# Kernel tuning notes

Hardware: AMD Instinct MI355X
Metric: run time of the kernel (lower is better)

The kernel has to match this reference:

```python
import jax, jax.numpy as jnp
import numpy as np

N = 50000      # nodes
E = 800000     # edges (avg degree 16)
D_IN = 128
D_H = 128
D_OUT = 64


def setup_inputs() -> dict:
    key = jax.random.key(0)
    k_x, k_e, k_w1, k_b1, k_w2, k_b2 = jax.random.split(key, 6)
    x = jax.random.normal(k_x, (N, D_IN), dtype=jnp.float32)
    edge_index = jax.random.randint(k_e, (2, E), 0, N, dtype=jnp.int32)
    # Glorot-style init for GCN weights, zero bias (as in PyG GCNConv defaults)
    W1 = jax.random.normal(k_w1, (D_IN, D_H), dtype=jnp.float32) * (1.0 / np.sqrt(D_IN))
    b1 = jnp.zeros((D_H,), dtype=jnp.float32)
    W2 = jax.random.normal(k_w2, (D_H, D_OUT), dtype=jnp.float32) * (1.0 / np.sqrt(D_H))
    b2 = jnp.zeros((D_OUT,), dtype=jnp.float32)
    return {"x": x, "edge_index": edge_index, "W1": W1, "b1": b1, "W2": W2, "b2": b2}


def _gcn_norm(edge_index, n):
    # PyG gcn_norm with add_self_loops=True, edge_weight = 1
    loops = jnp.arange(n, dtype=edge_index.dtype)
    src = jnp.concatenate([edge_index[0], loops])  # [E+N]
    dst = jnp.concatenate([edge_index[1], loops])
    deg = jax.ops.segment_sum(jnp.ones_like(dst, dtype=jnp.float32), dst, num_segments=n)
    dinv = jnp.where(deg > 0, jax.lax.rsqrt(deg), 0.0)
    norm = dinv[src] * dinv[dst]                   # [E+N]
    return src, dst, norm


def _gcn_conv(h, src, dst, norm, W, b, n):
    # transform -> gather source -> scale by symmetric norm -> scatter-add at dst -> bias
    hW = h @ W                                      # [N, F_out]
    msg = hW[src] * norm[:, None]                   # [E+N, F_out]
    agg = jax.ops.segment_sum(msg, dst, num_segments=n)
    return agg + b


def reference(x, edge_index, W1, b1, W2, b2):
    n = x.shape[0]
    src, dst, norm = _gcn_norm(edge_index, n)
    x1 = jax.nn.relu(_gcn_conv(x, src, dst, norm, W1, b1, n))
    x2 = _gcn_conv(x1, src, dst, norm, W2, b2, n)
    return x2
```

## Files before the change

kernel.cpp:

```cpp
#include <hip/hip_runtime.h>

#define CAP  64
#define BN   64
#define NBMAX 1024
#define ECAP 2048
#define P1E  4096

typedef unsigned int uint;
typedef unsigned short ushort;
typedef __attribute__((ext_vector_type(8))) short short8;
typedef __attribute__((ext_vector_type(4))) float f32x4;

__device__ inline ushort f2bf(float f) {
    uint u = __float_as_uint(f);
    return (ushort)((u + 0x7fffu + ((u >> 16) & 1u)) >> 16);
}
__device__ inline uint packbf2(float lo, float hi) {
    return (uint)f2bf(lo) | ((uint)f2bf(hi) << 16);
}
__device__ inline void unpackbf2(uint u, float& lo, float& hi) {
    lo = __uint_as_float(u << 16);
    hi = __uint_as_float(u & 0xffff0000u);
}

__global__ __launch_bounds__(256) void k_zero(uint4* __restrict__ p, int n16) {
    int i = blockIdx.x * 256 + threadIdx.x;
    if (i < n16) p[i] = make_uint4(0, 0, 0, 0);
}

__global__ __launch_bounds__(256) void k_part(const int* __restrict__ esrc,
                                              const int* __restrict__ edst,
                                              int E, int nb,
                                              int* __restrict__ gtail,
                                              uint* __restrict__ ebuf) {
    __shared__ int hist[NBMAX];
    int base_e = blockIdx.x * P1E;
    for (int i = threadIdx.x; i < nb; i += 256) hist[i] = 0;
    __syncthreads();

    int d[16], s[16];
#pragma unroll
    for (int u = 0; u < 16; u++) {
        int e = base_e + u * 256 + threadIdx.x;
        d[u] = (e < E) ? edst[e] : -1;
        s[u] = (e < E) ? esrc[e] : 0;
        if (d[u] >= 0) atomicAdd(&hist[d[u] >> 6], 1);
    }
    __syncthreads();

    for (int i = threadIdx.x; i < nb; i += 256) {
        int h = hist[i];
        hist[i] = (h > 0) ? atomicAdd(&gtail[i], h) : 0;
    }
    __syncthreads();

#pragma unroll
    for (int u = 0; u < 16; u++) {
        if (d[u] >= 0) {
            int b = d[u] >> 6;
            int slot = atomicAdd(&hist[b], 1);
            if (slot < ECAP)
                ebuf[(size_t)b * ECAP + slot] =
                    ((uint)(d[u] & (BN - 1)) << 16) | (uint)s[u];
        }
    }
}

__global__ __launch_bounds__(256) void k_csr(const uint* __restrict__ ebuf,
                                             const int* __restrict__ gtail,
                                             int n,
                                             ushort* __restrict__ colbuf,
                                             int* __restrict__ cnt,
                                             float* __restrict__ dinv) {
    __shared__ ushort cb[BN * CAP];
    __shared__ int cl[BN];
    int b = blockIdx.x;
    int ne = gtail[b];
    if (ne > ECAP) ne = ECAP;
    for (int i = threadIdx.x; i < BN; i += 256) cl[i] = 0;
    __syncthreads();

    const uint* eb = ebuf + (size_t)b * ECAP;
    for (int i = threadIdx.x; i < ne; i += 256) {
        uint pr = eb[i];
        int dloc = pr >> 16;
        int p = atomicAdd(&cl[dloc], 1);
        if (p < CAP) cb[dloc * CAP + p] = (ushort)(pr & 0xffffu);
    }
    __syncthreads();

    int node0 = b * BN;
    for (int i = threadIdx.x; i < BN * CAP / 8; i += 256) {
        int node = node0 + i / (CAP / 8);
        if (node < n)
            ((uint4*)&colbuf[(size_t)node0 * CAP])[i] = ((const uint4*)cb)[i];
    }
    for (int i = threadIdx.x; i < BN; i += 256) {
        int node = node0 + i;
        if (node < n) {
            int c = cl[i];
            dinv[node] = rsqrtf((float)c + 1.0f);
            cnt[node] = (c > CAP) ? CAP : c;
        }
    }
}

__global__ __launch_bounds__(256) void k_wprep(const float* __restrict__ W1,
                                               const float* __restrict__ W2,
                                               ushort* __restrict__ W1t,
                                               ushort* __restrict__ W2t) {
    int i = blockIdx.x * 256 + threadIdx.x;
    if (i < 4 * 128 * 32) {
        int kt = i >> 12;
        int nn = (i >> 5) & 127;
        int ko = i & 31;
        W1t[i] = f2bf(W1[(size_t)(kt * 32 + ko) * 128 + nn]);
    }
    int j = i - 4 * 128 * 32;
    if (j >= 0 && j < 4 * 64 * 32) {
        int kt = j >> 11;
        int nn = (j >> 5) & 63;
        int ko = j & 31;
        W2t[j] = f2bf(W2[(size_t)(kt * 32 + ko) * 64 + nn]);
    }
}

template<int NCOL, bool XF32>
__global__ __launch_bounds__(256) void k_mgemm(const float* __restrict__ Xf,
                                               const ushort* __restrict__ Xh,
                                               const ushort* __restrict__ Wt,
                                               ushort* __restrict__ Yb, int n) {
    __shared__ ushort Ws[4 * NCOL * 32];
    for (int idx = threadIdx.x; idx < 4 * NCOL * 32 / 8; idx += 256)
        ((uint4*)Ws)[idx] = ((const uint4*)Wt)[idx];
    __syncthreads();

    int wid  = threadIdx.x >> 6;
    int l    = threadIdx.x & 63;
    int mrow = l & 15;
    int kgrp = l >> 4;
    int row16 = (blockIdx.x * 4 + wid) * 16;
    int r  = row16 + mrow;
    int rc = (r < n) ? r : (n - 1);

    f32x4 acc[NCOL / 16];
#pragma unroll
    for (int t = 0; t < NCOL / 16; t++) acc[t] = (f32x4){0.f, 0.f, 0.f, 0.f};

#pragma unroll
    for (int kt = 0; kt < 4; kt++) {
        short8 a;
        if (XF32) {
            const float* xp = &Xf[(size_t)rc * 128 + kt * 32 + kgrp * 8];
            float4 x0 = *(const float4*)xp;
            float4 x1 = *(const float4*)(xp + 4);
            a[0] = (short)f2bf(x0.x); a[1] = (short)f2bf(x0.y);
            a[2] = (short)f2bf(x0.z); a[3] = (short)f2bf(x0.w);
            a[4] = (short)f2bf(x1.x); a[5] = (short)f2bf(x1.y);
            a[6] = (short)f2bf(x1.z); a[7] = (short)f2bf(x1.w);
        } else {
            a = *(const short8*)&Xh[(size_t)rc * 128 + kt * 32 + kgrp * 8];
        }
#pragma unroll
        for (int t = 0; t < NCOL / 16; t++) {
            short8 b = *(const short8*)&Ws[((kt * NCOL) + t * 16 + mrow) * 32 + kgrp * 8];
            acc[t] = __builtin_amdgcn_mfma_f32_16x16x32_bf16(a, b, acc[t], 0, 0, 0);
        }
    }

    int orow = row16 + kgrp * 4;
#pragma unroll
    for (int t = 0; t < NCOL / 16; t++) {
#pragma unroll
        for (int q = 0; q < 4; q++) {
            int rr = orow + q;
            if (rr < n) Yb[(size_t)rr * NCOL + t * 16 + mrow] = f2bf(acc[t][q]);
        }
    }
}

__global__ __launch_bounds__(256) void k_agg1(const ushort* __restrict__ Hb,
                                              const int* __restrict__ cntc,
                                              const ushort* __restrict__ colbuf,
                                              const float* __restrict__ dinv,
                                              const float* __restrict__ b1,
                                              ushort* __restrict__ x1b, int n) {
    const int CH = 128, LPG = 16;
    int t    = blockIdx.x * 256 + threadIdx.x;
    int gid  = t / LPG;
    int lane = t % LPG;
    if (gid >= n) return;

    float di = dinv[gid];
    int c = cntc[gid];
    if (c > CAP) c = CAP;

    float acc[8];
#pragma unroll
    for (int k = 0; k < 8; k++) acc[k] = 0.f;

    const ushort* cb = colbuf + (size_t)gid * CAP;
    for (int j = 0; j < c; j += 8) {
        uint4 iv = *(const uint4*)(cb + j);
        int s[8];
        s[0] = iv.x & 0xffff; s[1] = iv.x >> 16;
        s[2] = iv.y & 0xffff; s[3] = iv.y >> 16;
        s[4] = iv.z & 0xffff; s[5] = iv.z >> 16;
        s[6] = iv.w & 0xffff; s[7] = iv.w >> 16;
#pragma unroll
        for (int u = 1; u < 8; u++) if (j + u >= c) s[u] = s[0];
        float w[8];
#pragma unroll
        for (int u = 0; u < 8; u++)
            w[u] = (j + u < c) ? dinv[s[u]] : 0.f;
        uint4 h[8];
#pragma unroll
        for (int u = 0; u < 8; u++)
            h[u] = *(const uint4*)(Hb + (size_t)s[u] * CH + lane * 8);
#pragma unroll
        for (int u = 0; u < 8; u++) {
            float f0, f1;
            unpackbf2(h[u].x, f0, f1); acc[0] += f0 * w[u]; acc[1] += f1 * w[u];
            unpackbf2(h[u].y, f0, f1); acc[2] += f0 * w[u]; acc[3] += f1 * w[u];
            unpackbf2(h[u].z, f0, f1); acc[4] += f0 * w[u]; acc[5] += f1 * w[u];
            unpackbf2(h[u].w, f0, f1); acc[6] += f0 * w[u]; acc[7] += f1 * w[u];
        }
    }

    uint4 aself = *(const uint4*)(Hb + (size_t)gid * CH + lane * 8);
    float sf[8];
    unpackbf2(aself.x, sf[0], sf[1]);
    unpackbf2(aself.y, sf[2], sf[3]);
    unpackbf2(aself.z, sf[4], sf[5]);
    unpackbf2(aself.w, sf[6], sf[7]);

    float4 bb0 = *(const float4*)&b1[lane * 8];
    float4 bb1 = *(const float4*)&b1[lane * 8 + 4];
    float bb[8] = {bb0.x, bb0.y, bb0.z, bb0.w, bb1.x, bb1.y, bb1.z, bb1.w};

    float xv[8];
#pragma unroll
    for (int k = 0; k < 8; k++)
        xv[k] = fmaxf((acc[k] + di * sf[k]) * di + bb[k], 0.f);

    uint up[4] = { packbf2(xv[0], xv[1]), packbf2(xv[2], xv[3]),
                   packbf2(xv[4], xv[5]), packbf2(xv[6], xv[7]) };
    *(uint4*)&x1b[(size_t)gid * CH + lane * 8] = *(uint4*)up;
}

__global__ __launch_bounds__(256) void k_agg2(const ushort* __restrict__ Hb,
                                              const int* __restrict__ cntc,
                                              const ushort* __restrict__ colbuf,
                                              const float* __restrict__ dinv,
                                              const float* __restrict__ b2,
                                              float* __restrict__ out, int n) {
    const int CH = 64, LPG = 8;
    int t    = blockIdx.x * 256 + threadIdx.x;
    int gid  = t / LPG;
    int lane = t % LPG;
    if (gid >= n) return;

    float di = dinv[gid];
    int c = cntc[gid];
    if (c > CAP) c = CAP;

    float acc[8];
#pragma unroll
    for (int k = 0; k < 8; k++) acc[k] = 0.f;

    const ushort* cb = colbuf + (size_t)gid * CAP;
    for (int j = 0; j < c; j += 8) {
        uint4 iv = *(const uint4*)(cb + j);
        int s[8];
        s[0] = iv.x & 0xffff; s[1] = iv.x >> 16;
        s[2] = iv.y & 0xffff; s[3] = iv.y >> 16;
        s[4] = iv.z & 0xffff; s[5] = iv.z >> 16;
        s[6] = iv.w & 0xffff; s[7] = iv.w >> 16;
#pragma unroll
        for (int u = 1; u < 8; u++) if (j + u >= c) s[u] = s[0];
        float w[8];
#pragma unroll
        for (int u = 0; u < 8; u++)
            w[u] = (j + u < c) ? dinv[s[u]] : 0.f;
        uint4 h[8];
#pragma unroll
        for (int u = 0; u < 8; u++)
            h[u] = *(const uint4*)(Hb + (size_t)s[u] * CH + lane * 8);
#pragma unroll
        for (int u = 0; u < 8; u++) {
            float f0, f1;
            unpackbf2(h[u].x, f0, f1); acc[0] += f0 * w[u]; acc[1] += f1 * w[u];
            unpackbf2(h[u].y, f0, f1); acc[2] += f0 * w[u]; acc[3] += f1 * w[u];
            unpackbf2(h[u].z, f0, f1); acc[4] += f0 * w[u]; acc[5] += f1 * w[u];
            unpackbf2(h[u].w, f0, f1); acc[6] += f0 * w[u]; acc[7] += f1 * w[u];
        }
    }

    uint4 aself = *(const uint4*)(Hb + (size_t)gid * CH + lane * 8);
    float sf[8];
    unpackbf2(aself.x, sf[0], sf[1]);
    unpackbf2(aself.y, sf[2], sf[3]);
    unpackbf2(aself.z, sf[4], sf[5]);
    unpackbf2(aself.w, sf[6], sf[7]);

    float4 bb0 = *(const float4*)&b2[lane * 8];
    float4 bb1 = *(const float4*)&b2[lane * 8 + 4];
    float bb[8] = {bb0.x, bb0.y, bb0.z, bb0.w, bb1.x, bb1.y, bb1.z, bb1.w};

    float o[8];
#pragma unroll
    for (int k = 0; k < 8; k++)
        o[k] = (acc[k] + di * sf[k]) * di + bb[k];

    float* dst = out + (size_t)gid * CH + lane * 8;
    *(float4*)dst       = make_float4(o[0], o[1], o[2], o[3]);
    *(float4*)(dst + 4) = make_float4(o[4], o[5], o[6], o[7]);
}

extern "C" void kernel_launch(void* const* d_in, const int* in_sizes, int n_in,
                              void* d_out, int out_size, void* d_ws, size_t ws_size,
                              hipStream_t stream) {
    const float* x  = (const float*)d_in[0];
    const int*   ei = (const int*)d_in[1];
    const float* W1 = (const float*)d_in[2];
    const float* b1 = (const float*)d_in[3];
    const float* W2 = (const float*)d_in[4];
    const float* b2 = (const float*)d_in[5];
    float* out = (float*)d_out;

    int N = in_sizes[0] / 128;
    int E = in_sizes[1] / 2;
    const int* esrc = ei;
    const int* edst = ei + E;

    int nb = (N + BN - 1) / BN;

    char* ws = (char*)d_ws;
    size_t off = 0;
    auto alloc = [&](size_t bytes) -> void* {
        off = (off + 255) & ~(size_t)255;
        void* p = ws + off;
        off += bytes;
        return p;
    };
    int*    gtail   = (int*)   alloc((size_t)NBMAX * 4);
    int*    cnt     = (int*)   alloc((size_t)N * 4);
    float*  dinv    = (float*) alloc((size_t)N * 4);
    uint*   ebuf    = (uint*)  alloc((size_t)nb * ECAP * 4);
    ushort* colbuf  = (ushort*)alloc((size_t)nb * BN * CAP * 2);
    ushort* hW1b    = (ushort*)alloc((size_t)N * 128 * 2);
    ushort* x1b     = (ushort*)alloc((size_t)N * 128 * 2);
    ushort* hW2b    = (ushort*)alloc((size_t)N * 64 * 2);
    ushort* W1t     = (ushort*)alloc((size_t)4 * 128 * 32 * 2);
    ushort* W2t     = (ushort*)alloc((size_t)4 * 64 * 32 * 2);

    k_zero<<<1, 256, 0, stream>>>((uint4*)gtail, NBMAX / 4);

    int nbP1 = (E + P1E - 1) / P1E;
    k_part<<<nbP1, 256, 0, stream>>>(esrc, edst, E, nb, gtail, ebuf);
    k_wprep<<<96, 256, 0, stream>>>(W1, W2, W1t, W2t);
    k_mgemm<128, true><<<(N + 63) / 64, 256, 0, stream>>>(x, nullptr, W1t, hW1b, N);
    k_csr<<<nb, 256, 0, stream>>>(ebuf, gtail, N, colbuf, cnt, dinv);

    k_agg1<<<((size_t)N * 16 + 255) / 256, 256, 0, stream>>>(
        hW1b, cnt, colbuf, dinv, b1, x1b, N);

    k_mgemm<64, false><<<(N + 63) / 64, 256, 0, stream>>>(nullptr, x1b, W2t, hW2b, N);

    k_agg2<<<((size_t)N * 8 + 255) / 256, 256, 0, stream>>>(
        hW2b, cnt, colbuf, dinv, b2, out, N);
}
```

Measured before the change: 96.80 us.

## Fuse layer-1 aggregation with layer-2 GEMM and merge init kernels

The first aggregation kernel now writes its ReLU output tile of 64 nodes into swizzled shared memory. A 1024-thread block then runs the second-layer MFMA GEMM on that tile directly, so the x1 intermediate no longer goes to global memory and one kernel launch is dropped. The gtail zeroing and weight preparation kernels are also merged into a single init kernel. The larger blocks with a barrier may lower occupancy for the latency-bound gather, and colbuf gets padding to cover clamped reads.

```diff
diff --git a/kernel.cpp b/kernel.cpp
--- a/kernel.cpp
+++ b/kernel.cpp
@@ -23,9 +23,26 @@
     hi = __uint_as_float(u & 0xffff0000u);
 }
 
-__global__ __launch_bounds__(256) void k_zero(uint4* __restrict__ p, int n16) {
+__global__ __launch_bounds__(256) void k_init(const float* __restrict__ W1,
+                                              const float* __restrict__ W2,
+                                              ushort* __restrict__ W1t,
+                                              ushort* __restrict__ W2t,
+                                              int* __restrict__ gtail) {
     int i = blockIdx.x * 256 + threadIdx.x;
-    if (i < n16) p[i] = make_uint4(0, 0, 0, 0);
+    if (i < NBMAX) gtail[i] = 0;
+    if (i < 4 * 128 * 32) {
+        int kt = i >> 12;
+        int nn = (i >> 5) & 127;
+        int ko = i & 31;
+        W1t[i] = f2bf(W1[(size_t)(kt * 32 + ko) * 128 + nn]);
+    }
+    int j = i - 4 * 128 * 32;
+    if (j >= 0 && j < 4 * 64 * 32) {
+        int kt = j >> 11;
+        int nn = (j >> 5) & 63;
+        int ko = j & 31;
+        W2t[j] = f2bf(W2[(size_t)(kt * 32 + ko) * 64 + nn]);
+    }
 }
 
 __global__ __launch_bounds__(256) void k_part(const int* __restrict__ esrc,
@@ -105,33 +122,11 @@
     }
 }
 
-__global__ __launch_bounds__(256) void k_wprep(const float* __restrict__ W1,
-                                               const float* __restrict__ W2,
-                                               ushort* __restrict__ W1t,
-                                               ushort* __restrict__ W2t) {
-    int i = blockIdx.x * 256 + threadIdx.x;
-    if (i < 4 * 128 * 32) {
-        int kt = i >> 12;
-        int nn = (i >> 5) & 127;
-        int ko = i & 31;
-        W1t[i] = f2bf(W1[(size_t)(kt * 32 + ko) * 128 + nn]);
-    }
-    int j = i - 4 * 128 * 32;
-    if (j >= 0 && j < 4 * 64 * 32) {
-        int kt = j >> 11;
-        int nn = (j >> 5) & 63;
-        int ko = j & 31;
-        W2t[j] = f2bf(W2[(size_t)(kt * 32 + ko) * 64 + nn]);
-    }
-}
-
-template<int NCOL, bool XF32>
-__global__ __launch_bounds__(256) void k_mgemm(const float* __restrict__ Xf,
-                                               const ushort* __restrict__ Xh,
-                                               const ushort* __restrict__ Wt,
-                                               ushort* __restrict__ Yb, int n) {
-    __shared__ ushort Ws[4 * NCOL * 32];
-    for (int idx = threadIdx.x; idx < 4 * NCOL * 32 / 8; idx += 256)
+__global__ __launch_bounds__(256) void k_mgemm1(const float* __restrict__ Xf,
+                                                const ushort* __restrict__ Wt,
+                                                ushort* __restrict__ Yb, int n) {
+    __shared__ ushort Ws[4 * 128 * 32];
+    for (int idx = threadIdx.x; idx < 4 * 128 * 32 / 8; idx += 256)
         ((uint4*)Ws)[idx] = ((const uint4*)Wt)[idx];
     __syncthreads();
 
@@ -143,63 +138,65 @@
     int r  = row16 + mrow;
     int rc = (r < n) ? r : (n - 1);
 
-    f32x4 acc[NCOL / 16];
-#pragma unroll
-    for (int t = 0; t < NCOL / 16; t++) acc[t] = (f32x4){0.f, 0.f, 0.f, 0.f};
+    f32x4 acc[8];
+#pragma unroll
+    for (int t = 0; t < 8; t++) acc[t] = (f32x4){0.f, 0.f, 0.f, 0.f};
 
 #pragma unroll
     for (int kt = 0; kt < 4; kt++) {
+        const float* xp = &Xf[(size_t)rc * 128 + kt * 32 + kgrp * 8];
+        float4 x0 = *(const float4*)xp;
+        float4 x1 = *(const float4*)(xp + 4);
         short8 a;
-        if (XF32) {
-            const float* xp = &Xf[(size_t)rc * 128 + kt * 32 + kgrp * 8];
-            float4 x0 = *(const float4*)xp;
-            float4 x1 = *(const float4*)(xp + 4);
-            a[0] = (short)f2bf(x0.x); a[1] = (short)f2bf(x0.y);
-            a[2] = (short)f2bf(x0.z); a[3] = (short)f2bf(x0.w);
-            a[4] = (short)f2bf(x1.x); a[5] = (short)f2bf(x1.y);
-            a[6] = (short)f2bf(x1.z); a[7] = (short)f2bf(x1.w);
-        } else {
-            a = *(const short8*)&Xh[(size_t)rc * 128 + kt * 32 + kgrp * 8];
-        }
-#pragma unroll
-        for (int t = 0; t < NCOL / 16; t++) {
-            short8 b = *(const short8*)&Ws[((kt * NCOL) + t * 16 + mrow) * 32 + kgrp * 8];
+        a[0] = (short)f2bf(x0.x); a[1] = (short)f2bf(x0.y);
+        a[2] = (short)f2bf(x0.z); a[3] = (short)f2bf(x0.w);
+        a[4] = (short)f2bf(x1.x); a[5] = (short)f2bf(x1.y);
+        a[6] = (short)f2bf(x1.z); a[7] = (short)f2bf(x1.w);
+#pragma unroll
+        for (int t = 0; t < 8; t++) {
+            short8 b = *(const short8*)&Ws[((kt * 128) + t * 16 + mrow) * 32 + kgrp * 8];
             acc[t] = __builtin_amdgcn_mfma_f32_16x16x32_bf16(a, b, acc[t], 0, 0, 0);
         }
     }
 
     int orow = row16 + kgrp * 4;
 #pragma unroll
-    for (int t = 0; t < NCOL / 16; t++) {
+    for (int t = 0; t < 8; t++) {
 #pragma unroll
         for (int q = 0; q < 4; q++) {
             int rr = orow + q;
-            if (rr < n) Yb[(size_t)rr * NCOL + t * 16 + mrow] = f2bf(acc[t][q]);
-        }
-    }
-}
-
-__global__ __launch_bounds__(256) void k_agg1(const ushort* __restrict__ Hb,
-                                              const int* __restrict__ cntc,
-                                              const ushort* __restrict__ colbuf,
-                                              const float* __restrict__ dinv,
-                                              const float* __restrict__ b1,
-                                              ushort* __restrict__ x1b, int n) {
+            if (rr < n) Yb[(size_t)rr * 128 + t * 16 + mrow] = f2bf(acc[t][q]);
+        }
+    }
+}
+
+__global__ __launch_bounds__(1024) void k_agg1m(const ushort* __restrict__ Hb,
+                                                const int* __restrict__ cntc,
+                                                const ushort* __restrict__ colbuf,
+                                                const float* __restrict__ dinv,
+                                                const float* __restrict__ b1,
+                                                const ushort* __restrict__ W2t,
+                                                ushort* __restrict__ Yb2, int n) {
+    __shared__ ushort x1s[64 * 128];
+    __shared__ ushort Ws[4 * 64 * 32];
+    for (int idx = threadIdx.x; idx < 4 * 64 * 32 / 8; idx += 1024)
+        ((uint4*)Ws)[idx] = ((const uint4*)W2t)[idx];
+
     const int CH = 128, LPG = 16;
-    int t    = blockIdx.x * 256 + threadIdx.x;
-    int gid  = t / LPG;
-    int lane = t % LPG;
-    if (gid >= n) return;
-
-    float di = dinv[gid];
-    int c = cntc[gid];
+    int grp  = threadIdx.x / LPG;
+    int lane = threadIdx.x % LPG;
+    int gid  = blockIdx.x * 64 + grp;
+    int gc   = (gid < n) ? gid : (n - 1);
+
+    float di = dinv[gc];
+    int c = cntc[gc];
     if (c > CAP) c = CAP;
 
     float acc[8];
 #pragma unroll
     for (int k = 0; k < 8; k++) acc[k] = 0.f;
 
-    const ushort* cb = colbuf + (size_t)gid * CAP;
+    const ushort* cb = colbuf + (size_t)gc * CAP;
     for (int j = 0; j < c; j += 8) {
         uint4 iv = *(const uint4*)(cb + j);
         int s[8];
@@ -227,7 +224,7 @@
         }
     }
 
-    uint4 aself = *(const uint4*)(Hb + (size_t)gid * CH + lane * 8);
+    uint4 aself = *(const uint4*)(Hb + (size_t)gc * CH + lane * 8);
     float sf[8];
     unpackbf2(aself.x, sf[0], sf[1]);
     unpackbf2(aself.y, sf[2], sf[3]);
@@ -245,7 +242,32 @@
 
     uint up[4] = { packbf2(xv[0], xv[1]), packbf2(xv[2], xv[3]),
                    packbf2(xv[4], xv[5]), packbf2(xv[6], xv[7]) };
-    *(uint4*)&x1b[(size_t)gid * CH + lane * 8] = *(uint4*)up;
+    int slot = lane ^ (grp & 7);
+    *(uint4*)&x1s[grp * 128 + slot * 8] = *(uint4*)up;
+
+    __syncthreads();
+
+    int wv = threadIdx.x >> 6;
+    int l  = threadIdx.x & 63;
+    int wr = wv >> 2, wc = wv & 3;
+    int mrow = l & 15, kgrp = l >> 4;
+    int arow = wr * 16 + mrow;
+
+    f32x4 a2 = (f32x4){0.f, 0.f, 0.f, 0.f};
+#pragma unroll
+    for (int kt = 0; kt < 4; kt++) {
+        int slotA = (kt * 4 + kgrp) ^ (arow & 7);
+        short8 a = *(const short8*)&x1s[arow * 128 + slotA * 8];
+        short8 b = *(const short8*)&Ws[((kt * 64) + wc * 16 + mrow) * 32 + kgrp * 8];
+        a2 = __builtin_amdgcn_mfma_f32_16x16x32_bf16(a, b, a2, 0, 0, 0);
+    }
+
+    int row0 = blockIdx.x * 64 + wr * 16 + kgrp * 4;
+#pragma unroll
+    for (int q = 0; q < 4; q++) {
+        int rr = row0 + q;
+        if (rr < n) Yb2[(size_t)rr * 64 + wc * 16 + mrow] = f2bf(a2[q]);
+    }
 }
 
 __global__ __launch_bounds__(256) void k_agg2(const ushort* __restrict__ Hb,
@@ -347,25 +369,20 @@
     int*    cnt     = (int*)   alloc((size_t)N * 4);
     float*  dinv    = (float*) alloc((size_t)N * 4);
     uint*   ebuf    = (uint*)  alloc((size_t)nb * ECAP * 4);
-    ushort* colbuf  = (ushort*)alloc((size_t)nb * BN * CAP * 2);
+    ushort* colbuf  = (ushort*)alloc((size_t)nb * BN * CAP * 2 + 256);
     ushort* hW1b    = (ushort*)alloc((size_t)N * 128 * 2);
-    ushort* x1b     = (ushort*)alloc((size_t)N * 128 * 2);
     ushort* hW2b    = (ushort*)alloc((size_t)N * 64 * 2);
     ushort* W1t     = (ushort*)alloc((size_t)4 * 128 * 32 * 2);
     ushort* W2t     = (ushort*)alloc((size_t)4 * 64 * 32 * 2);
 
-    k_zero<<<1, 256, 0, stream>>>((uint4*)gtail, NBMAX / 4);
+    k_init<<<96, 256, 0, stream>>>(W1, W2, W1t, W2t, gtail);
 
     int nbP1 = (E + P1E - 1) / P1E;
     k_part<<<nbP1, 256, 0, stream>>>(esrc, edst, E, nb, gtail, ebuf);
-    k_wprep<<<96, 256, 0, stream>>>(W1, W2, W1t, W2t);
-    k_mgemm<128, true><<<(N + 63) / 64, 256, 0, stream>>>(x, nullptr, W1t, hW1b, N);
+    k_mgemm1<<<(N + 63) / 64, 256, 0, stream>>>(x, W1t, hW1b, N);
     k_csr<<<nb, 256, 0, stream>>>(ebuf, gtail, N, colbuf, cnt, dinv);
 
-    k_agg1<<<((size_t)N * 16 + 255) / 256, 256, 0, stream>>>(
-        hW1b, cnt, colbuf, dinv, b1, x1b, N);
-
-    k_mgemm<64, false><<<(N + 63) / 64, 256, 0, stream>>>(nullptr, x1b, W2t, hW2b, N);
+    k_agg1m<<<nb, 1024, 0, stream>>>(hW1b, cnt, colbuf, dinv, b1, W2t, hW2b, N);
 
     k_agg2<<<((size_t)N * 8 + 255) / 256, 256, 0, stream>>>(
         hW2b, cnt, colbuf, dinv, b2, out, N);
```

Result: no change. 98.08 us (+1.3%).
